# Performance work log

Hardware: AMD Instinct MI355X
Metric: run time of the kernel (lower is better)

Reference implementation:

```python
import jax, jax.numpy as jnp
import numpy as np

B_BLK = 64      # sparse_block_size
LOCAL = 4       # sparse_local_num_blocks
GLOB = 2        # sparse_global_num_blocks
STRIDE = 4      # sparse_global_block_stride
NH = 16
NKV = 4
HD = 128
SCALE = HD ** -0.5
NEG = -1e9


def _build_block_index(num_blocks):
    """Static per-query-block key-block index table + validity mask."""
    max_sel = LOCAL + 1 + GLOB
    idx = np.zeros((num_blocks, max_sel), np.int32)
    valid = np.zeros((num_blocks, max_sel), bool)
    for t in range(num_blocks):
        local = list(range(max(0, t - LOCAL), t + 1))
        cand = list(range(0, t + 1, max(1, STRIDE)))
        glob = cand[-GLOB:] if (GLOB > 0 and len(cand) > 0) else []
        sel = sorted(set(local + glob))
        idx[t, :len(sel)] = sel
        valid[t, :len(sel)] = True
    return idx, valid


def _rotate_half(x):
    x1, x2 = jnp.split(x, 2, axis=-1)
    return jnp.concatenate((-x2, x1), axis=-1)


def setup_inputs() -> dict:
    key = jax.random.key(0)
    ks = jax.random.split(key, 7)
    bsz, S, H = 1, 4096, 2048
    return {
        "hidden_states": jax.random.normal(ks[0], (bsz, S, H), jnp.float32) * 0.02,
        "cos": jax.random.uniform(ks[1], (bsz, S, HD), jnp.float32, -1.0, 1.0),
        "sin": jax.random.uniform(ks[2], (bsz, S, HD), jnp.float32, -1.0, 1.0),
        "wq": jax.random.normal(ks[3], (NH * HD, H), jnp.float32) * 0.02,
        "wk": jax.random.normal(ks[4], (NKV * HD, H), jnp.float32) * 0.02,
        "wv": jax.random.normal(ks[5], (NKV * HD, H), jnp.float32) * 0.02,
        "wo": jax.random.normal(ks[6], (H, NH * HD), jnp.float32) * 0.02,
    }


def reference(hidden_states, cos, sin, wq, wk, wv, wo):
    b, S, H = hidden_states.shape
    # QKV projections (nn.Linear: x @ W.T), split heads -> [b, h, S, d]
    q = (hidden_states @ wq.T).reshape(b, S, NH, HD).transpose(0, 2, 1, 3)
    k = (hidden_states @ wk.T).reshape(b, S, NKV, HD).transpose(0, 2, 1, 3)
    v = (hidden_states @ wv.T).reshape(b, S, NKV, HD).transpose(0, 2, 1, 3)
    # RoPE (cos/sin broadcast over heads)
    c = cos[:, None, :, :]
    s = sin[:, None, :, :]
    q = q * c + _rotate_half(q) * s
    k = k * c + _rotate_half(k) * s
    # GQA: repeat KV heads
    n_rep = NH // NKV
    k = jnp.repeat(k, n_rep, axis=1)
    v = jnp.repeat(v, n_rep, axis=1)
    # Block-sparse local+global attention (S divisible by B_BLK -> no padding)
    T = S // B_BLK
    q_blk = q.reshape(b, NH, T, B_BLK, HD)
    k_blk = k.reshape(b, NH, T, B_BLK, HD)
    v_blk = v.reshape(b, NH, T, B_BLK, HD)
    idx, valid = _build_block_index(T)           # [T, Smax] static
    Smax = idx.shape[1]
    k_sel = k_blk[:, :, idx]                     # [b,h,T,Smax,Bk,d]
    v_sel = v_blk[:, :, idx]
    scores = jnp.einsum('bhtqd,bhtspd->bhtqsp', q_blk, k_sel) * SCALE
    # causal intra-block mask on the diagonal block, -inf on padded slots
    intra = jnp.triu(jnp.full((B_BLK, B_BLK), NEG, jnp.float32), 1)
    is_diag = jnp.asarray(idx == np.arange(T)[:, None], jnp.float32)  # [T,Smax]
    mask = is_diag[:, None, :, None] * intra[None, :, None, :]        # [T,Bq,Smax,Bk]
    mask = mask + jnp.where(jnp.asarray(valid)[:, None, :, None], 0.0, NEG)
    scores = scores + mask[None, None]
    scores = scores.reshape(b, NH, T, B_BLK, Smax * B_BLK)
    probs = jax.nn.softmax(scores, axis=-1)
    out = jnp.einsum('bhtqk,bhtkd->bhtqd', probs,
                     v_sel.reshape(b, NH, T, Smax * B_BLK, HD))
    out = out.reshape(b, NH, S, HD).transpose(0, 2, 1, 3).reshape(b, S, NH * HD)
    return out @ wo.T
```

## Files before the change

### kernel.cpp

```cpp
#include <hip/hip_runtime.h>

typedef unsigned short u16;
typedef short bf16x8 __attribute__((ext_vector_type(8)));
typedef float f32x4 __attribute__((ext_vector_type(4)));

#define S_LEN 4096
#define NHEADS 16
#define NKVH 4
#define HDIM 128
#define HID 2048
#define NQKV 3072

__device__ __forceinline__ u16 f2bf(float x) {
  union { float f; unsigned u; } v; v.f = x;
  unsigned r = v.u + 0x7fffu + ((v.u >> 16) & 1u);
  return (u16)(r >> 16);
}
__device__ __forceinline__ float bf2f(u16 x) {
  union { unsigned u; float f; } v; v.u = ((unsigned)x) << 16;
  return v.f;
}
__device__ __forceinline__ void async16(u16* lds, const u16* g) {
  __builtin_amdgcn_global_load_lds((const __attribute__((address_space(1))) void*)g,
                                   (__attribute__((address_space(3))) void*)lds, 16, 0, 0);
}

__global__ __launch_bounds__(256) void cast_f32_bf16(const float* __restrict__ in,
                                                     u16* __restrict__ out, int n4) {
  int i = blockIdx.x * 256 + threadIdx.x;
  if (i >= n4) return;
  float4 v = ((const float4*)in)[i];
  ushort4 o;
  o.x = f2bf(v.x); o.y = f2bf(v.y); o.z = f2bf(v.z); o.w = f2bf(v.w);
  ((ushort4*)out)[i] = o;
}

template<bool OUT_BF16>
__global__ __launch_bounds__(256) void gemm_bt(const u16* __restrict__ A, const u16* __restrict__ B,
                                               void* __restrict__ Cp, int M, int N, int K) {
  __shared__ __align__(16) u16 As[128 * 64];
  __shared__ __align__(16) u16 Bs[128 * 64];
  const int tid = threadIdx.x;
  const int w = tid >> 6, l = tid & 63;
  const int quad = l >> 4, l16 = l & 15;
  const int bm = blockIdx.x, bn = blockIdx.y;
  const int wr = w & 1, wc = w >> 1;

  const size_t abase = (size_t)bm * 128 * K;
  const size_t bbase = (size_t)bn * 128 * K;

  f32x4 acc[4][4];
  for (int i = 0; i < 4; ++i)
    for (int j = 0; j < 4; ++j) acc[i][j] = f32x4{0.f, 0.f, 0.f, 0.f};

  int sm[4], sc[4];
  for (int j = 0; j < 4; ++j) {
    int slot = (w * 4 + j) * 64 + l;
    sm[j] = slot >> 3;
    sc[j] = (slot & 7) ^ (sm[j] & 7);
  }
  int aoff[2][4], boff[2][4];
  for (int ksi = 0; ksi < 2; ++ksi) {
    int cb = ksi * 4 + quad;
    for (int mt = 0; mt < 4; ++mt) {
      int m = wr * 64 + mt * 16 + l16;
      aoff[ksi][mt] = (m * 8 + (cb ^ (m & 7))) * 8;
      int n = wc * 64 + mt * 16 + l16;
      boff[ksi][mt] = (n * 8 + (cb ^ (n & 7))) * 8;
    }
  }

  for (int kt = 0; kt < K; kt += 64) {
    __syncthreads();
    for (int j = 0; j < 4; ++j) {
      async16(&As[(w * 4 + j) * 64 * 8], A + abase + (size_t)sm[j] * K + kt + sc[j] * 8);
      async16(&Bs[(w * 4 + j) * 64 * 8], B + bbase + (size_t)sm[j] * K + kt + sc[j] * 8);
    }
    __syncthreads();
    for (int ksi = 0; ksi < 2; ++ksi) {
      bf16x8 af[4], bv[4];
      for (int mt = 0; mt < 4; ++mt) {
        af[mt] = *(const bf16x8*)&As[aoff[ksi][mt]];
        bv[mt] = *(const bf16x8*)&Bs[boff[ksi][mt]];
      }
      for (int mt = 0; mt < 4; ++mt)
        for (int nt = 0; nt < 4; ++nt)
          acc[mt][nt] = __builtin_amdgcn_mfma_f32_16x16x32_bf16(af[mt], bv[nt], acc[mt][nt], 0, 0, 0);
    }
  }

  const int row_base = bm * 128 + wr * 64;
  const int col_base = bn * 128 + wc * 64;
  for (int mt = 0; mt < 4; ++mt)
    for (int nt = 0; nt < 4; ++nt) {
      int col = col_base + nt * 16 + l16;
      for (int r = 0; r < 4; ++r) {
        int row = row_base + mt * 16 + quad * 4 + r;
        float v = acc[mt][nt][r];
        if (OUT_BF16) ((u16*)Cp)[(size_t)row * N + col] = f2bf(v);
        else          ((float*)Cp)[(size_t)row * N + col] = v;
      }
    }
}

__global__ __launch_bounds__(256) void rope_scatter(const u16* __restrict__ qkv,
                                                    const float* __restrict__ cosp,
                                                    const float* __restrict__ sinp,
                                                    u16* __restrict__ Q, u16* __restrict__ Kd) {
  int idx = blockIdx.x * 256 + threadIdx.x;
  int d = idx & 63;
  int hh = (idx >> 6) % 20;
  int s = idx / (20 * 64);
  size_t base = (size_t)s * NQKV + hh * 128;
  float x1 = bf2f(qkv[base + d]);
  float x2 = bf2f(qkv[base + d + 64]);
  float c1 = cosp[s * 128 + d], s1 = sinp[s * 128 + d];
  float c2 = cosp[s * 128 + d + 64], s2 = sinp[s * 128 + d + 64];
  float o1 = x1 * c1 - x2 * s1;
  float o2 = x2 * c2 + x1 * s2;
  u16* dst = (hh < NHEADS) ? (Q + ((size_t)hh * S_LEN + s) * HDIM)
                           : (Kd + ((size_t)(hh - NHEADS) * S_LEN + s) * HDIM);
  dst[d] = f2bf(o1);
  dst[d + 64] = f2bf(o2);
}

__global__ __launch_bounds__(256) void vtrans(const u16* __restrict__ qkv, u16* __restrict__ Vt) {
  __shared__ u16 tile[64][65];
  int s0 = blockIdx.x * 64;
  int j0 = blockIdx.y * 64;
  int tid = threadIdx.x;
  for (int it = 0; it < 16; ++it) {
    int lin = it * 256 + tid;
    int sr = lin >> 6, jc = lin & 63;
    tile[sr][jc] = qkv[(size_t)(s0 + sr) * NQKV + 2560 + j0 + jc];
  }
  __syncthreads();
  for (int it = 0; it < 16; ++it) {
    int lin = it * 256 + tid;
    int dr = lin >> 6, sc = lin & 63;
    Vt[(size_t)(j0 + dr) * S_LEN + s0 + sc] = tile[sc][dr];
  }
}

__global__ __launch_bounds__(256) void attn_kernel(const u16* __restrict__ Q, const u16* __restrict__ K,
                                                   const u16* __restrict__ Vt, u16* __restrict__ Aout) {
  const float SCALE = 0.08838834764831845f;
  const float NEGF = -3.0e38f;
  const int t = blockIdx.x, h = blockIdx.y;
  const int kvh = h >> 2;
  const int tid = threadIdx.x;
  const int w = tid >> 6, l = tid & 63, quad = l >> 4, l16 = l & 15;

  __shared__ __align__(16) u16 Qs[64 * 128];
  __shared__ __align__(16) u16 Ks[64 * 128];
  __shared__ __align__(16) u16 Vs[128 * 64];
  __shared__ __align__(16) u16 Ps[4 * 16 * 72];

  int sel[7]; int nsel = 0;
  {
    int g1 = (t >> 2) << 2, g0 = g1 - 4;
    int lo = t - 4; if (lo < 0) lo = 0;
    if (g0 >= 0 && g0 < lo) sel[nsel++] = g0;
    if (g1 < lo) sel[nsel++] = g1;
    for (int b = lo; b <= t; ++b) sel[nsel++] = b;
  }

  {
    const size_t qbase = ((size_t)h * S_LEN + t * 64) * HDIM;
    for (int j = 0; j < 4; ++j) {
      int slot = (w * 4 + j) * 64 + l;
      int m = slot >> 4;
      int c = (slot & 15) ^ (m & 15);
      async16(&Qs[(w * 4 + j) * 64 * 8], Q + qbase + m * 128 + c * 8);
    }
  }

  float m_run[4], l_run[4];
  for (int r = 0; r < 4; ++r) { m_run[r] = NEGF; l_run[r] = 0.f; }
  f32x4 oacc[8];
  for (int i = 0; i < 8; ++i) oacc[i] = f32x4{0.f, 0.f, 0.f, 0.f};

  for (int ib = 0; ib < nsel; ++ib) {
    const int kb = sel[ib];
    __syncthreads();
    {
      const size_t kbase = ((size_t)kvh * S_LEN + kb * 64) * HDIM;
      const size_t vbase = (size_t)kvh * HDIM * S_LEN + kb * 64;
      for (int j = 0; j < 4; ++j) {
        int slot = (w * 4 + j) * 64 + l;
        int mk = slot >> 4;
        int ck = (slot & 15) ^ (mk & 15);
        async16(&Ks[(w * 4 + j) * 64 * 8], K + kbase + mk * 128 + ck * 8);
        int dv = slot >> 3;
        int cv = (slot & 7) ^ (dv & 7);
        async16(&Vs[(w * 4 + j) * 64 * 8], Vt + vbase + (size_t)dv * S_LEN + cv * 8);
      }
    }
    __syncthreads();

    f32x4 sacc[4];
    for (int nt = 0; nt < 4; ++nt) sacc[nt] = f32x4{0.f, 0.f, 0.f, 0.f};
    const int mq = w * 16 + l16;
    for (int ks = 0; ks < 128; ks += 32) {
      int cb = (ks >> 3) + quad;
      bf16x8 af = *(const bf16x8*)&Qs[(mq * 16 + (cb ^ (mq & 15))) * 8];
      for (int nt = 0; nt < 4; ++nt) {
        int n = nt * 16 + l16;
        bf16x8 bv = *(const bf16x8*)&Ks[(n * 16 + (cb ^ (n & 15))) * 8];
        sacc[nt] = __builtin_amdgcn_mfma_f32_16x16x32_bf16(af, bv, sacc[nt], 0, 0, 0);
      }
    }

    const bool diag = (kb == t);
    float alpha[4];
    for (int r = 0; r < 4; ++r) {
      int qrow = w * 16 + quad * 4 + r;
      float pv[4];
      float vmax = NEGF;
      for (int nt = 0; nt < 4; ++nt) {
        float v = sacc[nt][r] * SCALE;
        if (diag && (nt * 16 + l16) > qrow) v = NEGF;
        pv[nt] = v;
        vmax = fmaxf(vmax, v);
      }
      for (int off = 1; off < 16; off <<= 1) vmax = fmaxf(vmax, __shfl_xor(vmax, off));
      float mnew = fmaxf(m_run[r], vmax);
      alpha[r] = __expf(m_run[r] - mnew);
      m_run[r] = mnew;
      float sum = 0.f;
      for (int nt = 0; nt < 4; ++nt) {
        float p = __expf(pv[nt] - mnew);
        sum += p;
        Ps[(w * 16 + quad * 4 + r) * 72 + nt * 16 + l16] = f2bf(p);
      }
      for (int off = 1; off < 16; off <<= 1) sum += __shfl_xor(sum, off);
      l_run[r] = l_run[r] * alpha[r] + sum;
    }
    for (int nt = 0; nt < 8; ++nt) {
      f32x4 o = oacc[nt];
      o[0] *= alpha[0]; o[1] *= alpha[1]; o[2] *= alpha[2]; o[3] *= alpha[3];
      oacc[nt] = o;
    }

    for (int ks = 0; ks < 64; ks += 32) {
      bf16x8 pf = *(const bf16x8*)&Ps[(w * 16 + l16) * 72 + ks + quad * 8];
      int cb = (ks >> 3) + quad;
      for (int nt = 0; nt < 8; ++nt) {
        int n = nt * 16 + l16;
        bf16x8 vv = *(const bf16x8*)&Vs[(n * 8 + (cb ^ (n & 7))) * 8];
        oacc[nt] = __builtin_amdgcn_mfma_f32_16x16x32_bf16(pf, vv, oacc[nt], 0, 0, 0);
      }
    }
  }

  float inv[4];
  for (int r = 0; r < 4; ++r) inv[r] = 1.f / l_run[r];
  const int srow = t * 64 + w * 16 + quad * 4;
  for (int nt = 0; nt < 8; ++nt) {
    int col = h * 128 + nt * 16 + l16;
    for (int r = 0; r < 4; ++r)
      Aout[(size_t)(srow + r) * HID + col] = f2bf(oacc[nt][r] * inv[r]);
  }
}

extern "C" void kernel_launch(void* const* d_in, const int* in_sizes, int n_in,
                              void* d_out, int out_size, void* d_ws, size_t ws_size,
                              hipStream_t stream) {
  const float* hs   = (const float*)d_in[0];
  const float* cosp = (const float*)d_in[1];
  const float* sinp = (const float*)d_in[2];
  const float* wq   = (const float*)d_in[3];
  const float* wk   = (const float*)d_in[4];
  const float* wv   = (const float*)d_in[5];
  const float* wo   = (const float*)d_in[6];

  u16* hsb = (u16*)d_ws;
  u16* W   = hsb + (size_t)S_LEN * HID;
  u16* wob = W + (size_t)NQKV * HID;
  u16* qkv = wob + (size_t)HID * HID;
  u16* Qm  = qkv + (size_t)S_LEN * NQKV;
  u16* Km  = Qm + (size_t)NHEADS * S_LEN * HDIM;
  u16* Vt  = Km + (size_t)NKVH * S_LEN * HDIM;
  u16* att = Vt + (size_t)NKVH * HDIM * S_LEN;

  cast_f32_bf16<<<8192, 256, 0, stream>>>(hs, hsb, 2097152);
  cast_f32_bf16<<<4096, 256, 0, stream>>>(wq, W, 1048576);
  cast_f32_bf16<<<1024, 256, 0, stream>>>(wk, W + (size_t)4194304, 262144);
  cast_f32_bf16<<<1024, 256, 0, stream>>>(wv, W + (size_t)5242880, 262144);
  cast_f32_bf16<<<4096, 256, 0, stream>>>(wo, wob, 1048576);

  gemm_bt<true><<<dim3(32, 24), 256, 0, stream>>>(hsb, W, (void*)qkv, 4096, 3072, 2048);
  rope_scatter<<<20480, 256, 0, stream>>>(qkv, cosp, sinp, Qm, Km);
  vtrans<<<dim3(64, 8), 256, 0, stream>>>(qkv, Vt);
  attn_kernel<<<dim3(64, 16), 256, 0, stream>>>(Qm, Km, Vt, att);
  gemm_bt<false><<<dim3(32, 16), 256, 0, stream>>>(att, wob, d_out, 4096, 2048, 2048);
}
```

Measured before the change: 289.3 us.

## Merge cast and RoPE/V-transpose launches, vectorize RoPE, swizzle P buffer

Folds the five f32-to-bf16 cast launches into one kernel, and merges RoPE scatter with the V transpose into a single launch. The RoPE path now processes four elements per thread with vector loads and stores. In attention, the P scratch buffer uses an XOR-swizzled layout instead of padding, and the softmax row reductions are batched across rows so the shuffles interleave. These cut launch overhead and memory instructions, at the cost of more index arithmetic and a branchy multi-role kernel.

```diff
diff --git a/kernel.cpp b/kernel.cpp
--- a/kernel.cpp
+++ b/kernel.cpp
@@ -25,14 +25,25 @@
                                    (__attribute__((address_space(3))) void*)lds, 16, 0, 0);
 }
 
-__global__ __launch_bounds__(256) void cast_f32_bf16(const float* __restrict__ in,
-                                                     u16* __restrict__ out, int n4) {
+__global__ __launch_bounds__(256) void cast_all(const float* __restrict__ hs,
+                                                const float* __restrict__ wq,
+                                                const float* __restrict__ wk,
+                                                const float* __restrict__ wv,
+                                                const float* __restrict__ wo,
+                                                u16* __restrict__ hsb,
+                                                u16* __restrict__ W,
+                                                u16* __restrict__ wob) {
   int i = blockIdx.x * 256 + threadIdx.x;
-  if (i >= n4) return;
-  float4 v = ((const float4*)in)[i];
+  const float* src; u16* dst; int off;
+  if (i < 2097152)      { src = hs; dst = hsb;             off = i; }
+  else if (i < 3145728) { src = wq; dst = W;               off = i - 2097152; }
+  else if (i < 3407872) { src = wk; dst = W + 4194304;     off = i - 3145728; }
+  else if (i < 3670016) { src = wv; dst = W + 5242880;     off = i - 3407872; }
+  else                  { src = wo; dst = wob;             off = i - 3670016; }
+  float4 v = ((const float4*)src)[off];
   ushort4 o;
   o.x = f2bf(v.x); o.y = f2bf(v.y); o.z = f2bf(v.z); o.w = f2bf(v.w);
-  ((ushort4*)out)[i] = o;
+  ((ushort4*)dst)[off] = o;
 }
 
 template<bool OUT_BF16>
@@ -103,42 +114,55 @@
     }
 }
 
-__global__ __launch_bounds__(256) void rope_scatter(const u16* __restrict__ qkv,
-                                                    const float* __restrict__ cosp,
-                                                    const float* __restrict__ sinp,
-                                                    u16* __restrict__ Q, u16* __restrict__ Kd) {
-  int idx = blockIdx.x * 256 + threadIdx.x;
-  int d = idx & 63;
-  int hh = (idx >> 6) % 20;
-  int s = idx / (20 * 64);
-  size_t base = (size_t)s * NQKV + hh * 128;
-  float x1 = bf2f(qkv[base + d]);
-  float x2 = bf2f(qkv[base + d + 64]);
-  float c1 = cosp[s * 128 + d], s1 = sinp[s * 128 + d];
-  float c2 = cosp[s * 128 + d + 64], s2 = sinp[s * 128 + d + 64];
-  float o1 = x1 * c1 - x2 * s1;
-  float o2 = x2 * c2 + x1 * s2;
-  u16* dst = (hh < NHEADS) ? (Q + ((size_t)hh * S_LEN + s) * HDIM)
-                           : (Kd + ((size_t)(hh - NHEADS) * S_LEN + s) * HDIM);
-  dst[d] = f2bf(o1);
-  dst[d + 64] = f2bf(o2);
-}
-
-__global__ __launch_bounds__(256) void vtrans(const u16* __restrict__ qkv, u16* __restrict__ Vt) {
-  __shared__ u16 tile[64][65];
-  int s0 = blockIdx.x * 64;
-  int j0 = blockIdx.y * 64;
-  int tid = threadIdx.x;
-  for (int it = 0; it < 16; ++it) {
-    int lin = it * 256 + tid;
-    int sr = lin >> 6, jc = lin & 63;
-    tile[sr][jc] = qkv[(size_t)(s0 + sr) * NQKV + 2560 + j0 + jc];
-  }
-  __syncthreads();
-  for (int it = 0; it < 16; ++it) {
-    int lin = it * 256 + tid;
-    int dr = lin >> 6, sc = lin & 63;
-    Vt[(size_t)(j0 + dr) * S_LEN + s0 + sc] = tile[sc][dr];
+__global__ __launch_bounds__(256) void prep_kv(const u16* __restrict__ qkv,
+                                               const float* __restrict__ cosp,
+                                               const float* __restrict__ sinp,
+                                               u16* __restrict__ Q, u16* __restrict__ Kd,
+                                               u16* __restrict__ Vt) {
+  if (blockIdx.x < 5120) {
+    int idx = blockIdx.x * 256 + threadIdx.x;
+    int d4 = idx & 15;
+    int hh = (idx >> 4) % 20;
+    int s = idx / 320;
+    size_t base = (size_t)s * NQKV + hh * 128 + d4 * 4;
+    ushort4 x1 = *(const ushort4*)&qkv[base];
+    ushort4 x2 = *(const ushort4*)&qkv[base + 64];
+    const float* cb = cosp + s * 128 + d4 * 4;
+    const float* sb = sinp + s * 128 + d4 * 4;
+    float4 c1 = *(const float4*)cb;
+    float4 s1 = *(const float4*)sb;
+    float4 c2 = *(const float4*)(cb + 64);
+    float4 s2 = *(const float4*)(sb + 64);
+    ushort4 o1, o2;
+    o1.x = f2bf(bf2f(x1.x) * c1.x - bf2f(x2.x) * s1.x);
+    o1.y = f2bf(bf2f(x1.y) * c1.y - bf2f(x2.y) * s1.y);
+    o1.z = f2bf(bf2f(x1.z) * c1.z - bf2f(x2.z) * s1.z);
+    o1.w = f2bf(bf2f(x1.w) * c1.w - bf2f(x2.w) * s1.w);
+    o2.x = f2bf(bf2f(x2.x) * c2.x + bf2f(x1.x) * s2.x);
+    o2.y = f2bf(bf2f(x2.y) * c2.y + bf2f(x1.y) * s2.y);
+    o2.z = f2bf(bf2f(x2.z) * c2.z + bf2f(x1.z) * s2.z);
+    o2.w = f2bf(bf2f(x2.w) * c2.w + bf2f(x1.w) * s2.w);
+    u16* dst = (hh < NHEADS) ? (Q + ((size_t)hh * S_LEN + s) * HDIM)
+                             : (Kd + ((size_t)(hh - NHEADS) * S_LEN + s) * HDIM);
+    *(ushort4*)&dst[d4 * 4] = o1;
+    *(ushort4*)&dst[64 + d4 * 4] = o2;
+  } else {
+    __shared__ u16 tile[64][65];
+    int bb = blockIdx.x - 5120;
+    int s0 = (bb & 63) * 64;
+    int j0 = (bb >> 6) * 64;
+    int tid = threadIdx.x;
+    for (int it = 0; it < 16; ++it) {
+      int lin = it * 256 + tid;
+      int sr = lin >> 6, jc = lin & 63;
+      tile[sr][jc] = qkv[(size_t)(s0 + sr) * NQKV + 2560 + j0 + jc];
+    }
+    __syncthreads();
+    for (int it = 0; it < 16; ++it) {
+      int lin = it * 256 + tid;
+      int dr = lin >> 6, sc = lin & 63;
+      Vt[(size_t)(j0 + dr) * S_LEN + s0 + sc] = tile[sc][dr];
+    }
   }
 }
 
@@ -154,7 +178,7 @@
   __shared__ __align__(16) u16 Qs[64 * 128];
   __shared__ __align__(16) u16 Ks[64 * 128];
   __shared__ __align__(16) u16 Vs[128 * 64];
-  __shared__ __align__(16) u16 Ps[4 * 16 * 72];
+  __shared__ __align__(16) u16 Ps[4 * 16 * 64];
 
   int sel[7]; int nsel = 0;
   {
@@ -179,6 +203,8 @@
   for (int r = 0; r < 4; ++r) { m_run[r] = NEGF; l_run[r] = 0.f; }
   f32x4 oacc[8];
   for (int i = 0; i < 8; ++i) oacc[i] = f32x4{0.f, 0.f, 0.f, 0.f};
+
+  const int wbase = w * 16 * 64;
 
   for (int ib = 0; ib < nsel; ++ib) {
     const int kb = sel[ib];
@@ -212,30 +238,49 @@
     }
 
     const bool diag = (kb == t);
-    float alpha[4];
+    float pv[4][4];
+    #pragma unroll
+    for (int nt = 0; nt < 4; ++nt) {
+      int coln = nt * 16 + l16;
+      #pragma unroll
+      for (int r = 0; r < 4; ++r) {
+        float v = sacc[nt][r] * SCALE;
+        if (diag && coln > (w * 16 + quad * 4 + r)) v = NEGF;
+        pv[r][nt] = v;
+      }
+    }
+    float vmax[4];
+    #pragma unroll
+    for (int r = 0; r < 4; ++r)
+      vmax[r] = fmaxf(fmaxf(pv[r][0], pv[r][1]), fmaxf(pv[r][2], pv[r][3]));
+    #pragma unroll
+    for (int off = 1; off < 16; off <<= 1)
+      #pragma unroll
+      for (int r = 0; r < 4; ++r) vmax[r] = fmaxf(vmax[r], __shfl_xor(vmax[r], off));
+    float alpha[4], sum[4];
+    #pragma unroll
     for (int r = 0; r < 4; ++r) {
-      int qrow = w * 16 + quad * 4 + r;
-      float pv[4];
-      float vmax = NEGF;
-      for (int nt = 0; nt < 4; ++nt) {
-        float v = sacc[nt][r] * SCALE;
-        if (diag && (nt * 16 + l16) > qrow) v = NEGF;
-        pv[nt] = v;
-        vmax = fmaxf(vmax, v);
-      }
-      for (int off = 1; off < 16; off <<= 1) vmax = fmaxf(vmax, __shfl_xor(vmax, off));
-      float mnew = fmaxf(m_run[r], vmax);
+      float mnew = fmaxf(m_run[r], vmax[r]);
       alpha[r] = __expf(m_run[r] - mnew);
       m_run[r] = mnew;
-      float sum = 0.f;
+      sum[r] = 0.f;
+      int rl = quad * 4 + r;
+      #pragma unroll
       for (int nt = 0; nt < 4; ++nt) {
-        float p = __expf(pv[nt] - mnew);
-        sum += p;
-        Ps[(w * 16 + quad * 4 + r) * 72 + nt * 16 + l16] = f2bf(p);
-      }
-      for (int off = 1; off < 16; off <<= 1) sum += __shfl_xor(sum, off);
-      l_run[r] = l_run[r] * alpha[r] + sum;
-    }
+        float p = __expf(pv[r][nt] - mnew);
+        sum[r] += p;
+        int col = nt * 16 + l16;
+        Ps[wbase + (rl * 8 + ((col >> 3) ^ (rl & 7))) * 8 + (col & 7)] = f2bf(p);
+      }
+    }
+    #pragma unroll
+    for (int off = 1; off < 16; off <<= 1)
+      #pragma unroll
+      for (int r = 0; r < 4; ++r) sum[r] += __shfl_xor(sum[r], off);
+    #pragma unroll
+    for (int r = 0; r < 4; ++r) l_run[r] = l_run[r] * alpha[r] + sum[r];
+
+    #pragma unroll
     for (int nt = 0; nt < 8; ++nt) {
       f32x4 o = oacc[nt];
       o[0] *= alpha[0]; o[1] *= alpha[1]; o[2] *= alpha[2]; o[3] *= alpha[3];
@@ -243,7 +288,7 @@
     }
 
     for (int ks = 0; ks < 64; ks += 32) {
-      bf16x8 pf = *(const bf16x8*)&Ps[(w * 16 + l16) * 72 + ks + quad * 8];
+      bf16x8 pf = *(const bf16x8*)&Ps[wbase + (l16 * 8 + ((quad + (ks >> 3)) ^ (l16 & 7))) * 8];
       int cb = (ks >> 3) + quad;
       for (int nt = 0; nt < 8; ++nt) {
         int n = nt * 16 + l16;
@@ -283,15 +328,9 @@
   u16* Vt  = Km + (size_t)NKVH * S_LEN * HDIM;
   u16* att = Vt + (size_t)NKVH * HDIM * S_LEN;
 
-  cast_f32_bf16<<<8192, 256, 0, stream>>>(hs, hsb, 2097152);
-  cast_f32_bf16<<<4096, 256, 0, stream>>>(wq, W, 1048576);
-  cast_f32_bf16<<<1024, 256, 0, stream>>>(wk, W + (size_t)4194304, 262144);
-  cast_f32_bf16<<<1024, 256, 0, stream>>>(wv, W + (size_t)5242880, 262144);
-  cast_f32_bf16<<<4096, 256, 0, stream>>>(wo, wob, 1048576);
-
+  cast_all<<<18432, 256, 0, stream>>>(hs, wq, wk, wv, wo, hsb, W, wob);
   gemm_bt<true><<<dim3(32, 24), 256, 0, stream>>>(hsb, W, (void*)qkv, 4096, 3072, 2048);
-  rope_scatter<<<20480, 256, 0, stream>>>(qkv, cosp, sinp, Qm, Km);
-  vtrans<<<dim3(64, 8), 256, 0, stream>>>(qkv, Vt);
+  prep_kv<<<5632, 256, 0, stream>>>(qkv, cosp, sinp, Qm, Km, Vt);
   attn_kernel<<<dim3(64, 16), 256, 0, stream>>>(Qm, Km, Vt, att);
   gemm_bt<false><<<dim3(32, 16), 256, 0, stream>>>(att, wob, d_out, 4096, 2048, 2048);
 }
```

Result: no change. 291.6 us (+0.8%).
